# Kernel tuning notes

Hardware: AMD Instinct MI355X
Metric: run time of the kernel (lower is better)

## Reference

```python
import jax, jax.numpy as jnp
import numpy as np

BS = 1024
D = 64            # hidden_dim
S = 16            # neighbor_samples
HOPS = 2          # context_hops
AGG = 1.0         # agg_param
N_ENT = 200000
N_EDGE = 2000000
N_REL = 16


def setup_inputs() -> dict:
    key = jax.random.key(0)
    ks = jax.random.split(key, 10)
    return {
        "relations":    jax.random.randint(ks[0], (BS,), 0, N_REL),
        "entity_pairs": jax.random.randint(ks[1], (BS, 2), 0, N_ENT),
        "train_edges":  jax.random.randint(ks[2], (BS,), 0, N_EDGE),
        "entity2edges": jax.random.randint(ks[3], (N_ENT, S), 0, N_EDGE),
        "edge2entities": jax.random.randint(ks[4], (N_EDGE, 2), 0, N_ENT),
        "edge2relation": jax.random.randint(ks[5], (N_EDGE,), 0, N_REL),
        "relation_emb": jax.random.normal(ks[6], (N_REL, D), jnp.float32) * (1.0 / D ** 0.5),
        "entity_emb":   jax.random.normal(ks[7], (N_ENT, D), jnp.float32) * (1.0 / D ** 0.5),
        "scorer_w":     jax.random.normal(ks[8], (D, 1), jnp.float32) * 0.1,
        "scorer_b":     jnp.zeros((1,), jnp.float32),
    }


def reference(relations, entity_pairs, train_edges, entity2edges, edge2entities,
              edge2relation, relation_emb, entity_emb, scorer_w, scorer_b):
    bs = relations.shape[0]
    dtype = relation_emb.dtype

    # ---- _get_entity_neighbors_and_masks (train mode) ----
    edges_list = [relations]          # hop-0 "edges" are the relation ids
    nodes_list = []
    mask_list = []
    te = train_edges[:, None]         # the edge to predict is masked out
    for i in range(HOPS):
        if i == 0:
            neighbor_entities = entity_pairs                      # [bs, 2]
        else:
            # entities at the two endpoints of every previous-hop edge
            neighbor_entities = edge2entities[edges_list[-1]].reshape(bs, -1, 2)
        nodes_list.append(neighbor_entities)
        neighbor_edges = entity2edges[neighbor_entities.reshape(bs, -1)].reshape(bs, -1)
        edges_list.append(neighbor_edges)
        mask_list.append((neighbor_edges != te).astype(dtype))    # (edge - train_edge) != 0

    # ---- embedding lookups ----
    entity_vectors = [entity_emb[n] for n in nodes_list]
    edge_vectors = [relation_emb[edges_list[0]]]                  # [bs, D]
    for edges in edges_list[1:]:
        edge_vectors.append(relation_emb[edge2relation[edges]])

    # ---- iterative MeanAggregator hops (self_included=True) ----
    for i in range(HOPS):
        next_edge_vectors = []
        for hop in range(HOPS - i):
            self_vec = edge_vectors[hop].reshape(bs, -1, D)              # [bs, m, D]
            nev = entity_vectors[hop].reshape(bs, -1, 2, D)              # [bs, m, 2, D]
            nbv = edge_vectors[hop + 1].reshape(bs, -1, 2, S, D)         # [bs, m, 2, S, D]
            m = mask_list[hop].reshape(bs, -1, 2, S, 1)                  # [bs, m, 2, S, 1]
            nei_nums = jnp.sum(m, axis=-2)                               # [bs, m, 2, 1]
            nei_nums = jnp.where(nei_nums == 0, jnp.ones_like(nei_nums), nei_nums)
            edge_agg = jnp.sum(nbv * m, axis=-2) / nei_nums              # masked mean over S
            neighbor_vectors = nev + AGG * edge_agg                      # [bs, m, 2, D]
            self_vec = self_vec + AGG * jnp.mean(neighbor_vectors, axis=-2)
            next_edge_vectors.append(self_vec)
        edge_vectors = next_edge_vectors

    out = edge_vectors[0].reshape(bs, D)
    scores = out @ scorer_w + scorer_b                                   # mlp scorer
    return scores[:, 0]
```

## Files before the change

### kernel.cpp

```cpp
#include <hip/hip_runtime.h>


#define DIM 64
#define NS 16
#define NREL 16

__global__ __launch_bounds__(256) void pack_nib_kernel(
    const int* __restrict__ e2r, unsigned int* __restrict__ nib, int n) {
    const int tid = blockIdx.x * blockDim.x + threadIdx.x;
    const int i = tid * 8;
    if (i + 7 < n) {
        const int4 a = *reinterpret_cast<const int4*>(e2r + i);
        const int4 b = *reinterpret_cast<const int4*>(e2r + i + 4);
        unsigned int w =  (unsigned int)(a.x & 15)
                       | ((unsigned int)(a.y & 15) << 4)
                       | ((unsigned int)(a.z & 15) << 8)
                       | ((unsigned int)(a.w & 15) << 12)
                       | ((unsigned int)(b.x & 15) << 16)
                       | ((unsigned int)(b.y & 15) << 20)
                       | ((unsigned int)(b.z & 15) << 24)
                       | ((unsigned int)(b.w & 15) << 28);
        nib[tid] = w;
    } else if (i < n) {
        unsigned int w = 0;
        for (int k = 0; k < 8 && i + k < n; ++k)
            w |= ((unsigned int)(e2r[i + k] & 15)) << (4 * k);
        nib[tid] = w;
    }
}

__device__ __forceinline__ int rel4(const unsigned int* __restrict__ nib, int e) {
    return (int)((nib[e >> 3] >> ((e & 7) << 2)) & 15u);
}

__global__ __launch_bounds__(512, 8) void transmatch_main(
    const int* __restrict__ relations,
    const int* __restrict__ entity_pairs,
    const int* __restrict__ train_edges,
    const int* __restrict__ entity2edges,
    const int* __restrict__ edge2entities,
    const float* __restrict__ relation_emb,
    const float* __restrict__ entity_emb,
    const float* __restrict__ scorer_w,
    const float* __restrict__ scorer_b,
    const unsigned int* __restrict__ nib,
    float* __restrict__ out)
{
    __shared__ float RwL[NREL];
    __shared__ float wL[DIM];
    __shared__ int   node_l[64];
    __shared__ int   m0i[32];
    __shared__ float c0s[2];
    __shared__ float ews[2];
    __shared__ float rw0s[2];
    __shared__ float wavesum[8];

    const int b    = blockIdx.x;
    const int t    = threadIdx.x;
    const int lane = t & 63;
    const int wave = t >> 6;
    const int te   = train_edges[b];

    if (t < DIM) wL[t] = scorer_w[t];

    int rel1 = 0, m0 = 0;
    if (wave == 0 && lane < 32) {
        const int p    = lane >> 4;
        const int e    = entity_pairs[b * 2 + p];
        const int edge = entity2edges[e * NS + (lane & 15)];
        m0   = (edge != te) ? 1 : 0;
        rel1 = rel4(nib, edge);
        const int2 nn = reinterpret_cast<const int2*>(edge2entities)[edge];
        reinterpret_cast<int2*>(node_l)[lane] = nn;
        m0i[lane] = m0;
        int c = m0;
        c += __shfl_xor(c, 1); c += __shfl_xor(c, 2);
        c += __shfl_xor(c, 4); c += __shfl_xor(c, 8);
        if ((lane & 15) == 0) c0s[p] = (float)c;
    } else if (wave == 1) {
        const int p  = lane >> 5;
        const int e  = entity_pairs[b * 2 + p];
        const int k  = lane & 31;
        const float2 ev = reinterpret_cast<const float2*>(entity_emb)[e * 32 + k];
        float v = ev.x * scorer_w[2 * k] + ev.y * scorer_w[2 * k + 1];
        v += __shfl_xor(v, 1); v += __shfl_xor(v, 2); v += __shfl_xor(v, 4);
        v += __shfl_xor(v, 8); v += __shfl_xor(v, 16);
        if (k == 0) ews[p] = v;
    } else if (wave == 2) {
        const int r = lane >> 2, seg = lane & 3;
        const float4* R4 = reinterpret_cast<const float4*>(relation_emb);
        const float4* W4 = reinterpret_cast<const float4*>(scorer_w);
        float v = 0.0f;
        #pragma unroll
        for (int k = 0; k < 4; ++k) {
            const float4 rr = R4[r * 16 + seg * 4 + k];
            const float4 ww = W4[seg * 4 + k];
            v = fmaf(rr.x, ww.x, v); v = fmaf(rr.y, ww.y, v);
            v = fmaf(rr.z, ww.z, v); v = fmaf(rr.w, ww.w, v);
        }
        v += __shfl_xor(v, 1); v += __shfl_xor(v, 2);
        if (seg == 0) RwL[r] = v;
    }
    __syncthreads();

    if (wave == 0 && lane < 32) {
        float rv = m0 ? RwL[rel1] : 0.0f;
        rv += __shfl_xor(rv, 1); rv += __shfl_xor(rv, 2);
        rv += __shfl_xor(rv, 4); rv += __shfl_xor(rv, 8);
        if ((lane & 15) == 0) rw0s[lane >> 4] = rv;
    }

    {
        const int n    = t >> 3;
        const int h    = t & 7;
        const int node = node_l[n];

        const int2 ed = reinterpret_cast<const int2*>(entity2edges)[node * 8 + h];
        const int ra = rel4(nib, ed.x);
        const int rb = rel4(nib, ed.y);

        const float4* E4  = reinterpret_cast<const float4*>(entity_emb);
        const float4* wL4 = reinterpret_cast<const float4*>(wL);
        const float4 ev0 = E4[node * 16 + h * 2];
        const float4 ev1 = E4[node * 16 + h * 2 + 1];
        const float4 w0  = wL4[h * 2];
        const float4 w1  = wL4[h * 2 + 1];
        float dotp = 0.0f;
        dotp = fmaf(ev0.x, w0.x, dotp); dotp = fmaf(ev0.y, w0.y, dotp);
        dotp = fmaf(ev0.z, w0.z, dotp); dotp = fmaf(ev0.w, w0.w, dotp);
        dotp = fmaf(ev1.x, w1.x, dotp); dotp = fmaf(ev1.y, w1.y, dotp);
        dotp = fmaf(ev1.z, w1.z, dotp); dotp = fmaf(ev1.w, w1.w, dotp);

        int cnt = 0; float rws = 0.0f;
        if (ed.x != te) { cnt++; rws += RwL[ra]; }
        if (ed.y != te) { cnt++; rws += RwL[rb]; }

        dotp += __shfl_xor(dotp, 1); dotp += __shfl_xor(dotp, 2); dotp += __shfl_xor(dotp, 4);
        rws  += __shfl_xor(rws, 1);  rws  += __shfl_xor(rws, 2);  rws  += __shfl_xor(rws, 4);
        cnt  += __shfl_xor(cnt, 1);  cnt  += __shfl_xor(cnt, 2);  cnt  += __shfl_xor(cnt, 4);

        float v = 0.0f;
        if (h == 0 && m0i[n >> 1])
            v = dotp + rws / (float)max(cnt, 1);

        v += __shfl_xor(v, 8); v += __shfl_xor(v, 16); v += __shfl_xor(v, 32);
        if (lane == 0) wavesum[wave] = v;
    }
    __syncthreads();

    if (t == 0) {
        const float i0 = 1.0f / fmaxf(c0s[0], 1.0f);
        const float i1 = 1.0f / fmaxf(c0s[1], 1.0f);
        const float S0 = wavesum[0] + wavesum[1] + wavesum[2] + wavesum[3];
        const float S1 = wavesum[4] + wavesum[5] + wavesum[6] + wavesum[7];
        const int   r0 = relations[b];
        out[b] = scorer_b[0] + RwL[r0]
               + ews[0] + i0 * rw0s[0] + 0.25f * i0 * S0
               + ews[1] + i1 * rw0s[1] + 0.25f * i1 * S1;
    }
}

extern "C" void kernel_launch(void* const* d_in, const int* in_sizes, int n_in,
                              void* d_out, int out_size, void* d_ws, size_t ws_size,
                              hipStream_t stream) {
    const int*   relations     = (const int*)d_in[0];
    const int*   entity_pairs  = (const int*)d_in[1];
    const int*   train_edges   = (const int*)d_in[2];
    const int*   entity2edges  = (const int*)d_in[3];
    const int*   edge2entities = (const int*)d_in[4];
    const int*   edge2relation = (const int*)d_in[5];
    const float* relation_emb  = (const float*)d_in[6];
    const float* entity_emb    = (const float*)d_in[7];
    const float* scorer_w      = (const float*)d_in[8];
    const float* scorer_b      = (const float*)d_in[9];
    float* out = (float*)d_out;

    const int bs     = in_sizes[0];
    const int n_edge = in_sizes[5];
    const int n_words = (n_edge + 7) / 8;

    unsigned int* nib = (unsigned int*)d_ws;
    pack_nib_kernel<<<(n_words + 255) / 256, 256, 0, stream>>>(
        edge2relation, nib, n_edge);

    transmatch_main<<<bs, 512, 0, stream>>>(
        relations, entity_pairs, train_edges, entity2edges, edge2entities,
        relation_emb, entity_emb, scorer_w, scorer_b, nib, out);
}
```

Measured before the change: 20.56 us.

## Restructure main kernel to one wave per pair and precompute projections

Moves the relation-embedding and entity-pair scorer projections into the prologue kernel, which now also does the nibble packing, so the main kernel reads precomputed scalars. The main kernel now uses 256-thread blocks that handle two batch rows, with one wave per entity of the pair. Neighbor lists are shared through wave shuffles instead of LDS, and each lane handles 8 hop-2 edges. This removes one block-wide barrier and the per-block recomputation. In exchange each lane does more serial gathers and the launch grid has half as many blocks, assuming an even batch size.

```diff
diff --git a/kernel.cpp b/kernel.cpp
--- a/kernel.cpp
+++ b/kernel.cpp
@@ -5,158 +5,198 @@
 #define NS 16
 #define NREL 16
 
-__global__ __launch_bounds__(256) void pack_nib_kernel(
-    const int* __restrict__ e2r, unsigned int* __restrict__ nib, int n) {
-    const int tid = blockIdx.x * blockDim.x + threadIdx.x;
-    const int i = tid * 8;
-    if (i + 7 < n) {
-        const int4 a = *reinterpret_cast<const int4*>(e2r + i);
-        const int4 b = *reinterpret_cast<const int4*>(e2r + i + 4);
-        unsigned int w =  (unsigned int)(a.x & 15)
-                       | ((unsigned int)(a.y & 15) << 4)
-                       | ((unsigned int)(a.z & 15) << 8)
-                       | ((unsigned int)(a.w & 15) << 12)
-                       | ((unsigned int)(b.x & 15) << 16)
-                       | ((unsigned int)(b.y & 15) << 20)
-                       | ((unsigned int)(b.z & 15) << 24)
-                       | ((unsigned int)(b.w & 15) << 28);
-        nib[tid] = w;
-    } else if (i < n) {
-        unsigned int w = 0;
-        for (int k = 0; k < 8 && i + k < n; ++k)
-            w |= ((unsigned int)(e2r[i + k] & 15)) << (4 * k);
-        nib[tid] = w;
-    }
-}
-
 __device__ __forceinline__ int rel4(const unsigned int* __restrict__ nib, int e) {
     return (int)((nib[e >> 3] >> ((e & 7) << 2)) & 15u);
 }
 
-__global__ __launch_bounds__(512, 8) void transmatch_main(
+__global__ __launch_bounds__(256) void precompute_kernel(
+    const int* __restrict__ e2r,
+    const int* __restrict__ entity_pairs,
+    const float* __restrict__ relation_emb,
+    const float* __restrict__ entity_emb,
+    const float* __restrict__ scorer_w,
+    unsigned int* __restrict__ nib,
+    float* __restrict__ Rw,
+    float* __restrict__ EWp,
+    int n_edge, int n_pairs, int nib_blocks, int ew_blocks)
+{
+    const int blk = blockIdx.x;
+    const int t   = threadIdx.x;
+    if (blk < nib_blocks) {
+        const int tid = blk * 256 + t;
+        const int i = tid * 8;
+        if (i + 7 < n_edge) {
+            const int4 a = *reinterpret_cast<const int4*>(e2r + i);
+            const int4 b = *reinterpret_cast<const int4*>(e2r + i + 4);
+            nib[tid] =  (unsigned int)(a.x & 15)
+                     | ((unsigned int)(a.y & 15) << 4)
+                     | ((unsigned int)(a.z & 15) << 8)
+                     | ((unsigned int)(a.w & 15) << 12)
+                     | ((unsigned int)(b.x & 15) << 16)
+                     | ((unsigned int)(b.y & 15) << 20)
+                     | ((unsigned int)(b.z & 15) << 24)
+                     | ((unsigned int)(b.w & 15) << 28);
+        } else if (i < n_edge) {
+            unsigned int w = 0;
+            for (int k = 0; k < 8 && i + k < n_edge; ++k)
+                w |= ((unsigned int)(e2r[i + k] & 15)) << (4 * k);
+            nib[tid] = w;
+        }
+        return;
+    }
+    const int j = blk - nib_blocks;
+    const float4* W4 = reinterpret_cast<const float4*>(scorer_w);
+    if (j < ew_blocks) {
+        const int q   = j * 64 + (t >> 2);
+        const int seg = t & 3;
+        if (q < n_pairs) {
+            const int e = entity_pairs[q];
+            const float4* E4 = reinterpret_cast<const float4*>(entity_emb);
+            float v = 0.0f;
+            #pragma unroll
+            for (int k = 0; k < 4; ++k) {
+                const float4 a = E4[(size_t)e * 16 + seg * 4 + k];
+                const float4 w = W4[seg * 4 + k];
+                v = fmaf(a.x, w.x, v); v = fmaf(a.y, w.y, v);
+                v = fmaf(a.z, w.z, v); v = fmaf(a.w, w.w, v);
+            }
+            v += __shfl_xor(v, 1); v += __shfl_xor(v, 2);
+            if (seg == 0) EWp[q] = v;
+        }
+    } else if (j == ew_blocks) {
+        if (t < 64) {
+            const int r = t >> 2, seg = t & 3;
+            const float4* R4 = reinterpret_cast<const float4*>(relation_emb);
+            float v = 0.0f;
+            #pragma unroll
+            for (int k = 0; k < 4; ++k) {
+                const float4 a = R4[r * 16 + seg * 4 + k];
+                const float4 w = W4[seg * 4 + k];
+                v = fmaf(a.x, w.x, v); v = fmaf(a.y, w.y, v);
+                v = fmaf(a.z, w.z, v); v = fmaf(a.w, w.w, v);
+            }
+            v += __shfl_xor(v, 1); v += __shfl_xor(v, 2);
+            if (seg == 0) Rw[r] = v;
+        }
+    }
+}
+
+__global__ __launch_bounds__(256) void transmatch_main(
     const int* __restrict__ relations,
     const int* __restrict__ entity_pairs,
     const int* __restrict__ train_edges,
     const int* __restrict__ entity2edges,
     const int* __restrict__ edge2entities,
-    const float* __restrict__ relation_emb,
     const float* __restrict__ entity_emb,
     const float* __restrict__ scorer_w,
     const float* __restrict__ scorer_b,
     const unsigned int* __restrict__ nib,
+    const float* __restrict__ Rwg,
+    const float* __restrict__ EWp,
     float* __restrict__ out)
 {
-    __shared__ float RwL[NREL];
     __shared__ float wL[DIM];
-    __shared__ int   node_l[64];
-    __shared__ int   m0i[32];
-    __shared__ float c0s[2];
-    __shared__ float ews[2];
-    __shared__ float rw0s[2];
-    __shared__ float wavesum[8];
-
-    const int b    = blockIdx.x;
+    __shared__ float RwLds[NREL];
+    __shared__ float ewn_l[4][32];
+    __shared__ float part[4][4];
+
     const int t    = threadIdx.x;
     const int lane = t & 63;
-    const int wave = t >> 6;
-    const int te   = train_edges[b];
-
-    if (t < DIM) wL[t] = scorer_w[t];
-
-    int rel1 = 0, m0 = 0;
-    if (wave == 0 && lane < 32) {
-        const int p    = lane >> 4;
-        const int e    = entity_pairs[b * 2 + p];
-        const int edge = entity2edges[e * NS + (lane & 15)];
-        m0   = (edge != te) ? 1 : 0;
-        rel1 = rel4(nib, edge);
-        const int2 nn = reinterpret_cast<const int2*>(edge2entities)[edge];
-        reinterpret_cast<int2*>(node_l)[lane] = nn;
-        m0i[lane] = m0;
-        int c = m0;
-        c += __shfl_xor(c, 1); c += __shfl_xor(c, 2);
-        c += __shfl_xor(c, 4); c += __shfl_xor(c, 8);
-        if ((lane & 15) == 0) c0s[p] = (float)c;
-    } else if (wave == 1) {
-        const int p  = lane >> 5;
-        const int e  = entity_pairs[b * 2 + p];
-        const int k  = lane & 31;
-        const float2 ev = reinterpret_cast<const float2*>(entity_emb)[e * 32 + k];
-        float v = ev.x * scorer_w[2 * k] + ev.y * scorer_w[2 * k + 1];
-        v += __shfl_xor(v, 1); v += __shfl_xor(v, 2); v += __shfl_xor(v, 4);
-        v += __shfl_xor(v, 8); v += __shfl_xor(v, 16);
-        if (k == 0) ews[p] = v;
-    } else if (wave == 2) {
-        const int r = lane >> 2, seg = lane & 3;
-        const float4* R4 = reinterpret_cast<const float4*>(relation_emb);
-        const float4* W4 = reinterpret_cast<const float4*>(scorer_w);
-        float v = 0.0f;
-        #pragma unroll
-        for (int k = 0; k < 4; ++k) {
-            const float4 rr = R4[r * 16 + seg * 4 + k];
-            const float4 ww = W4[seg * 4 + k];
-            v = fmaf(rr.x, ww.x, v); v = fmaf(rr.y, ww.y, v);
-            v = fmaf(rr.z, ww.z, v); v = fmaf(rr.w, ww.w, v);
-        }
-        v += __shfl_xor(v, 1); v += __shfl_xor(v, 2);
-        if (seg == 0) RwL[r] = v;
-    }
-    __syncthreads();
-
-    if (wave == 0 && lane < 32) {
-        float rv = m0 ? RwL[rel1] : 0.0f;
-        rv += __shfl_xor(rv, 1); rv += __shfl_xor(rv, 2);
-        rv += __shfl_xor(rv, 4); rv += __shfl_xor(rv, 8);
-        if ((lane & 15) == 0) rw0s[lane >> 4] = rv;
-    }
+    const int wv   = t >> 6;
+    const int b    = blockIdx.x * 2 + (wv >> 1);
+    const int p    = wv & 1;
+
+    wL[lane] = scorer_w[lane];
+    if (lane < NREL) RwLds[lane] = Rwg[lane];
+
+    const int te  = train_edges[b];
+    const int e_p = entity_pairs[b * 2 + p];
+
+    int m0 = 0, nx = 0, ny = 0;
+    float rw1 = 0.0f;
+    if (lane < NS) {
+        const int edge_s = entity2edges[e_p * NS + lane];
+        m0 = (edge_s != te) ? 1 : 0;
+        const int rel1 = rel4(nib, edge_s);
+        rw1 = m0 ? RwLds[rel1] : 0.0f;
+        const int2 nn = reinterpret_cast<const int2*>(edge2entities)[edge_s];
+        nx = nn.x; ny = nn.y;
+    }
+    int   c0  = m0;
+    float rw0 = rw1;
+    c0  += __shfl_xor(c0, 1);  c0  += __shfl_xor(c0, 2);
+    c0  += __shfl_xor(c0, 4);  c0  += __shfl_xor(c0, 8);
+    rw0 += __shfl_xor(rw0, 1); rw0 += __shfl_xor(rw0, 2);
+    rw0 += __shfl_xor(rw0, 4); rw0 += __shfl_xor(rw0, 8);
+
+    const int srcl = lane >> 2;
+    const int ndx  = __shfl(nx, srcl);
+    const int ndy  = __shfl(ny, srcl);
+    const int node = ((lane >> 1) & 1) ? ndy : ndx;
+    const int m0n  = __shfl(m0, srcl);
+
+    const int4 ea = *reinterpret_cast<const int4*>(entity2edges + (size_t)node * NS + (lane & 1) * 8);
+    const int4 eb = *reinterpret_cast<const int4*>(entity2edges + (size_t)node * NS + (lane & 1) * 8 + 4);
+
+    const int r0_ = rel4(nib, ea.x), r1_ = rel4(nib, ea.y);
+    const int r2_ = rel4(nib, ea.z), r3_ = rel4(nib, ea.w);
+    const int r4_ = rel4(nib, eb.x), r5_ = rel4(nib, eb.y);
+    const int r6_ = rel4(nib, eb.z), r7_ = rel4(nib, eb.w);
+
+    float rws = 0.0f; int cnt = 0;
+    if (ea.x != te) { cnt++; rws += RwLds[r0_]; }
+    if (ea.y != te) { cnt++; rws += RwLds[r1_]; }
+    if (ea.z != te) { cnt++; rws += RwLds[r2_]; }
+    if (ea.w != te) { cnt++; rws += RwLds[r3_]; }
+    if (eb.x != te) { cnt++; rws += RwLds[r4_]; }
+    if (eb.y != te) { cnt++; rws += RwLds[r5_]; }
+    if (eb.z != te) { cnt++; rws += RwLds[r6_]; }
+    if (eb.w != te) { cnt++; rws += RwLds[r7_]; }
+    rws += __shfl_xor(rws, 1);
+    cnt += __shfl_xor(cnt, 1);
 
     {
-        const int n    = t >> 3;
-        const int h    = t & 7;
-        const int node = node_l[n];
-
-        const int2 ed = reinterpret_cast<const int2*>(entity2edges)[node * 8 + h];
-        const int ra = rel4(nib, ed.x);
-        const int rb = rel4(nib, ed.y);
-
         const float4* E4  = reinterpret_cast<const float4*>(entity_emb);
         const float4* wL4 = reinterpret_cast<const float4*>(wL);
-        const float4 ev0 = E4[node * 16 + h * 2];
-        const float4 ev1 = E4[node * 16 + h * 2 + 1];
-        const float4 w0  = wL4[h * 2];
-        const float4 w1  = wL4[h * 2 + 1];
-        float dotp = 0.0f;
-        dotp = fmaf(ev0.x, w0.x, dotp); dotp = fmaf(ev0.y, w0.y, dotp);
-        dotp = fmaf(ev0.z, w0.z, dotp); dotp = fmaf(ev0.w, w0.w, dotp);
-        dotp = fmaf(ev1.x, w1.x, dotp); dotp = fmaf(ev1.y, w1.y, dotp);
-        dotp = fmaf(ev1.z, w1.z, dotp); dotp = fmaf(ev1.w, w1.w, dotp);
-
-        int cnt = 0; float rws = 0.0f;
-        if (ed.x != te) { cnt++; rws += RwL[ra]; }
-        if (ed.y != te) { cnt++; rws += RwL[rb]; }
-
-        dotp += __shfl_xor(dotp, 1); dotp += __shfl_xor(dotp, 2); dotp += __shfl_xor(dotp, 4);
-        rws  += __shfl_xor(rws, 1);  rws  += __shfl_xor(rws, 2);  rws  += __shfl_xor(rws, 4);
-        cnt  += __shfl_xor(cnt, 1);  cnt  += __shfl_xor(cnt, 2);  cnt  += __shfl_xor(cnt, 4);
-
-        float v = 0.0f;
-        if (h == 0 && m0i[n >> 1])
-            v = dotp + rws / (float)max(cnt, 1);
-
-        v += __shfl_xor(v, 8); v += __shfl_xor(v, 16); v += __shfl_xor(v, 32);
-        if (lane == 0) wavesum[wave] = v;
+        const int c = lane & 15;
+        const float4 wc = wL4[c];
+        #pragma unroll
+        for (int q = 0; q < 8; ++q) {
+            const int row   = q * 4 + (lane >> 4);
+            const int nodeq = __shfl(node, row * 2);
+            const float4 ev = E4[(size_t)nodeq * 16 + c];
+            float v = 0.0f;
+            v = fmaf(ev.x, wc.x, v); v = fmaf(ev.y, wc.y, v);
+            v = fmaf(ev.z, wc.z, v); v = fmaf(ev.w, wc.w, v);
+            v += __shfl_xor(v, 1); v += __shfl_xor(v, 2);
+            v += __shfl_xor(v, 4); v += __shfl_xor(v, 8);
+            if (c == 0) ewn_l[wv][row] = v;
+        }
+    }
+
+    const float ewn = ewn_l[wv][lane >> 1];
+    float v = 0.0f;
+    if ((lane & 1) == 0 && m0n)
+        v = ewn + rws / (float)max(cnt, 1);
+    v += __shfl_xor(v, 2);  v += __shfl_xor(v, 4);
+    v += __shfl_xor(v, 8);  v += __shfl_xor(v, 16); v += __shfl_xor(v, 32);
+
+    if (lane == 0) {
+        part[wv][0] = v;
+        part[wv][1] = rw0;
+        part[wv][2] = (float)c0;
+        part[wv][3] = EWp[b * 2 + p];
     }
     __syncthreads();
 
-    if (t == 0) {
-        const float i0 = 1.0f / fmaxf(c0s[0], 1.0f);
-        const float i1 = 1.0f / fmaxf(c0s[1], 1.0f);
-        const float S0 = wavesum[0] + wavesum[1] + wavesum[2] + wavesum[3];
-        const float S1 = wavesum[4] + wavesum[5] + wavesum[6] + wavesum[7];
+    if ((wv & 1) == 0 && lane == 0) {
+        const int w0 = wv, w1 = wv + 1;
+        const float i0 = 1.0f / fmaxf(part[w0][2], 1.0f);
+        const float i1 = 1.0f / fmaxf(part[w1][2], 1.0f);
         const int   r0 = relations[b];
-        out[b] = scorer_b[0] + RwL[r0]
-               + ews[0] + i0 * rw0s[0] + 0.25f * i0 * S0
-               + ews[1] + i1 * rw0s[1] + 0.25f * i1 * S1;
+        out[b] = scorer_b[0] + RwLds[r0]
+               + part[w0][3] + i0 * part[w0][1] + 0.25f * i0 * part[w0][0]
+               + part[w1][3] + i1 * part[w1][1] + 0.25f * i1 * part[w1][0];
     }
 }
 
@@ -175,15 +215,23 @@
     const float* scorer_b      = (const float*)d_in[9];
     float* out = (float*)d_out;
 
-    const int bs     = in_sizes[0];
-    const int n_edge = in_sizes[5];
+    const int bs      = in_sizes[0];
+    const int n_pairs = in_sizes[1];
+    const int n_edge  = in_sizes[5];
     const int n_words = (n_edge + 7) / 8;
 
     unsigned int* nib = (unsigned int*)d_ws;
-    pack_nib_kernel<<<(n_words + 255) / 256, 256, 0, stream>>>(
-        edge2relation, nib, n_edge);
-
-    transmatch_main<<<bs, 512, 0, stream>>>(
+    const size_t RW_OFF = ((size_t)n_words * 4 + 255) & ~(size_t)255;
+    float* Rw  = (float*)((char*)d_ws + RW_OFF);
+    float* EWp = Rw + 64;
+
+    const int nib_blocks = (n_words + 255) / 256;
+    const int ew_blocks  = (n_pairs + 63) / 64;
+    precompute_kernel<<<nib_blocks + ew_blocks + 1, 256, 0, stream>>>(
+        edge2relation, entity_pairs, relation_emb, entity_emb, scorer_w,
+        nib, Rw, EWp, n_edge, n_pairs, nib_blocks, ew_blocks);
+
+    transmatch_main<<<bs / 2, 256, 0, stream>>>(
         relations, entity_pairs, train_edges, entity2edges, edge2entities,
-        relation_emb, entity_emb, scorer_w, scorer_b, nib, out);
-}
+        entity_emb, scorer_w, scorer_b, nib, Rw, EWp, out);
+}
```

Result: slower. 23.34 us (+13.5%).
